# Optimization experiments

Measured on AMD Instinct MI355X. Metric: run time of the kernel, lower is better.

## Reference

```python
import jax, jax.numpy as jnp
import numpy as np

B, C_IN, H, W = 2, 256, 64, 64
C_OUT, NUM_HEADS = 256, 8
HEAD_DIM = C_OUT // NUM_HEADS


def setup_inputs() -> dict:
    key = jax.random.key(0)
    k_x, k_wqkv, k_bqkv, k_wout, k_bout = jax.random.split(key, 5)
    s_in = 1.0 / np.sqrt(C_IN)
    s_out = 1.0 / np.sqrt(C_OUT)
    return {
        "x": jax.random.normal(k_x, (B, C_IN, H, W), dtype=jnp.float32),
        "W_qkv": jax.random.uniform(k_wqkv, (C_IN, 3 * C_OUT), dtype=jnp.float32, minval=-s_in, maxval=s_in),
        "b_qkv": jax.random.uniform(k_bqkv, (3 * C_OUT,), dtype=jnp.float32, minval=-s_in, maxval=s_in),
        "W_out": jax.random.uniform(k_wout, (C_OUT, C_OUT), dtype=jnp.float32, minval=-s_out, maxval=s_out),
        "b_out": jax.random.uniform(k_bout, (C_OUT,), dtype=jnp.float32, minval=-s_out, maxval=s_out),
    }


def reference(x, W_qkv, b_qkv, W_out, b_out):
    b, c, h, w = x.shape
    n = h * w
    # [B, C, H, W] -> [B, N, C]
    xt = x.reshape(b, c, n).transpose(0, 2, 1)
    qkv = xt @ W_qkv + b_qkv                      # [B, N, 3*C_OUT]
    qkv = qkv.reshape(b, n, 3, NUM_HEADS, HEAD_DIM)
    q = qkv[:, :, 0].transpose(0, 2, 1, 3)        # [B, H, N, dh]
    k = qkv[:, :, 1].transpose(0, 2, 1, 3)
    v = qkv[:, :, 2].transpose(0, 2, 1, 3)
    scale = 1.0 / np.sqrt(HEAD_DIM).astype(np.float32)
    attn = jnp.einsum('bhnd,bhmd->bhnm', q, k) * scale   # [B, H, N, N]
    attn = jax.nn.softmax(attn, axis=-1)
    out = jnp.einsum('bhnm,bhmd->bhnd', attn, v)          # [B, H, N, dh]
    out = out.transpose(0, 2, 1, 3).reshape(b, n, C_OUT)  # [B, N, C_OUT]
    out = out @ W_out + b_out
    # [B, N, C_OUT] -> [B, C_OUT, sqrt(N), sqrt(N)]
    return out.transpose(0, 2, 1).reshape(b, C_OUT, h, w)
```

## Files before the change

kernel.cpp:

```cpp
#include <hip/hip_runtime.h>

typedef _Float16 f16;
typedef _Float16 f16x2 __attribute__((ext_vector_type(2)));
typedef _Float16 f16x4 __attribute__((ext_vector_type(4)));
typedef _Float16 f16x8 __attribute__((ext_vector_type(8)));
typedef float f32x4 __attribute__((ext_vector_type(4)));
typedef float f32x16 __attribute__((ext_vector_type(16)));

#define NTOK 4096
#define CIN  256
#define C3   768
#define CO   256
#define NH   8
#define DH   32

__device__ __forceinline__ f32x4 mfma16(f16x8 a, f16x8 b, f32x4 c) {
  return __builtin_amdgcn_mfma_f32_16x16x32_f16(a, b, c, 0, 0, 0);
}
__device__ __forceinline__ f32x16 mfma32(f16x8 a, f16x8 b, f32x16 c) {
  return __builtin_amdgcn_mfma_f32_32x32x16_f16(a, b, c, 0, 0, 0);
}

__device__ __forceinline__ float fexp2(float x) {
  float r; asm("v_exp_f32 %0, %1" : "=v"(r) : "v"(x)); return r;
}

__device__ __forceinline__ f16x2 cvt_pk(float lo, float hi) {
  return __builtin_bit_cast(f16x2, __builtin_amdgcn_cvt_pkrtz(lo, hi));
}

__device__ __forceinline__ f16x8 pack8(float a0, float a1, float a2, float a3,
                                       float a4, float a5, float a6, float a7) {
  f16x2 p0 = cvt_pk(a0, a1);
  f16x2 p1 = cvt_pk(a2, a3);
  f16x2 p2 = cvt_pk(a4, a5);
  f16x2 p3 = cvt_pk(a6, a7);
  f16x4 lo = __builtin_shufflevector(p0, p1, 0, 1, 2, 3);
  f16x4 hi = __builtin_shufflevector(p2, p3, 0, 1, 2, 3);
  return __builtin_shufflevector(lo, hi, 0, 1, 2, 3, 4, 5, 6, 7);
}

__device__ __forceinline__ f16x8 ld8(const f16* p) {
  f16x4 lo = *reinterpret_cast<const f16x4*>(p);
  f16x4 hi = *reinterpret_cast<const f16x4*>(p + 4);
  return __builtin_shufflevector(lo, hi, 0, 1, 2, 3, 4, 5, 6, 7);
}

__global__ __launch_bounds__(256) void qkv_kernel(
    const float* __restrict__ x, const float* __restrict__ Wqkv,
    const float* __restrict__ bqkv,
    f16* __restrict__ qbuf, f16* __restrict__ kbuf, f16* __restrict__ vbuf)
{
  __shared__ f16 As[64][36];
  __shared__ f16 Bs[64][36];
  const int b  = blockIdx.z;
  const int n0 = blockIdx.x * 64;
  const int j0 = blockIdx.y * 64;
  const int t  = threadIdx.x;
  const int w  = t >> 6;
  const int lane = t & 63;
  const int l16  = lane & 15;
  const int g4   = lane >> 4;
  const int rowi = t & 63;
  const int cg   = (t >> 6) * 8;

  f32x4 acc[4] = {};
  for (int k0 = 0; k0 < CIN; k0 += 32) {
    float av[8], bv[8];
#pragma unroll
    for (int jj = 0; jj < 8; ++jj) {
      av[jj] = x[((size_t)b * CIN + (k0 + cg + jj)) * NTOK + n0 + rowi];
      bv[jj] = Wqkv[(size_t)(k0 + cg + jj) * C3 + j0 + rowi];
    }
    f16x4 alo, ahi, blo, bhi;
#pragma unroll
    for (int jj = 0; jj < 4; ++jj) {
      alo[jj] = (f16)av[jj];  ahi[jj] = (f16)av[jj + 4];
      blo[jj] = (f16)bv[jj];  bhi[jj] = (f16)bv[jj + 4];
    }
    *reinterpret_cast<f16x4*>(&As[rowi][cg])     = alo;
    *reinterpret_cast<f16x4*>(&As[rowi][cg + 4]) = ahi;
    *reinterpret_cast<f16x4*>(&Bs[rowi][cg])     = blo;
    *reinterpret_cast<f16x4*>(&Bs[rowi][cg + 4]) = bhi;
    __syncthreads();
    f16x8 bf = ld8(&Bs[w * 16 + l16][g4 * 8]);
#pragma unroll
    for (int mf = 0; mf < 4; ++mf) {
      f16x8 af = ld8(&As[mf * 16 + l16][g4 * 8]);
      acc[mf] = mfma16(af, bf, acc[mf]);
    }
    __syncthreads();
  }
  const int j  = j0 + w * 16 + l16;
  const int s  = j >> 8;
  const int hh = (j >> 5) & 7;
  const int d  = j & 31;
  const float bias = bqkv[j];
  const float qscale = 0.25503472f;
  const int bh = b * NH + hh;
#pragma unroll
  for (int mf = 0; mf < 4; ++mf) {
#pragma unroll
    for (int r = 0; r < 4; ++r) {
      const int n = n0 + mf * 16 + g4 * 4 + r;
      const float v = acc[mf][r] + bias;
      if (s == 0) {
        qbuf[((size_t)bh * NTOK + n) * DH + d] = (f16)(v * qscale);
      } else if (s == 1) {
        kbuf[((size_t)bh * NTOK + n) * DH + d] = (f16)v;
      } else {
        const int g4p  = ((g4 & 1) << 1) | (g4 >> 1);
        const int tile = (n0 >> 5) + (mf >> 1);
        const int pos  = ((mf & 1) << 4) + g4p * 4 + r;
        vbuf[((size_t)bh * (NTOK / 32) + tile) * (DH * 32) + d * 32 + pos] = (f16)v;
      }
    }
  }
}

__global__ __launch_bounds__(512) void attn_kernel(
    const f16* __restrict__ qbuf, const f16* __restrict__ kbuf,
    const f16* __restrict__ vbuf, f16* __restrict__ ao)
{
  __shared__ float po_lds[4][32][33];
  __shared__ float pl_lds[4][32];

  const int flat = blockIdx.x + (int)gridDim.x * blockIdx.y;
  const int nper = ((int)gridDim.x * (int)gridDim.y) >> 3;
  const int jj   = (flat & 7) * nper + (flat >> 3);
  const int bh = jj >> 5;
  const int q0 = (jj & 31) * 128;
  const int b = bh >> 3, h = bh & 7;
  const int t = threadIdx.x, w = t >> 6, lane = t & 63;
  const int wq = w & 3, z = w >> 2;
  const int l32 = lane & 31, hi = lane >> 5;
  const size_t kbase = (size_t)bh * NTOK * DH;

  const int qrow = q0 + wq * 32 + l32;
  const f16* qp = qbuf + kbase + (size_t)qrow * DH + hi * 8;
  const f16x8 qf0 = *reinterpret_cast<const f16x8*>(qp);
  const f16x8 qf1 = *reinterpret_cast<const f16x8*>(qp + 16);

  const size_t zoff = (size_t)z * 65536;
  const f16* kp = kbuf + kbase + zoff + (size_t)l32 * DH + hi * 8;
  const f16* vp = vbuf + kbase + zoff + (size_t)l32 * 32 + hi * 8;

  f32x16 oacc = {};
  float lrun = 0.f;
  const f32x16 zero = {};

  f16x8 kna, knb, vca, vcb, vna, vnb;
  f32x16 scur;
  {
    f16x8 k0a = *reinterpret_cast<const f16x8*>(kp);
    f16x8 k0b = *reinterpret_cast<const f16x8*>(kp + 16);
    vca = *reinterpret_cast<const f16x8*>(vp);
    vcb = *reinterpret_cast<const f16x8*>(vp + 16);
    kna = *reinterpret_cast<const f16x8*>(kp + 1024);
    knb = *reinterpret_cast<const f16x8*>(kp + 1024 + 16);
    vna = *reinterpret_cast<const f16x8*>(vp + 1024);
    vnb = *reinterpret_cast<const f16x8*>(vp + 1024 + 16);
    scur = mfma32(k0a, qf0, zero);
    scur = mfma32(k0b, qf1, scur);
  }

  const f16* kfut = kp + 2048;
  const f16* vfut = vp + 2048;

#pragma unroll 2
  for (int tt = 0; tt < 64; ++tt) {
    f16x8 kpa = *reinterpret_cast<const f16x8*>(kfut);
    f16x8 kpb = *reinterpret_cast<const f16x8*>(kfut + 16);
    f16x8 vpa = *reinterpret_cast<const f16x8*>(vfut);
    f16x8 vpb = *reinterpret_cast<const f16x8*>(vfut + 16);
    kfut += 1024; vfut += 1024;

    __builtin_amdgcn_s_setprio(1);
    f32x16 snext = mfma32(kna, qf0, zero);
    snext = mfma32(knb, qf1, snext);
    __builtin_amdgcn_s_setprio(0);

    float e[16];
#pragma unroll
    for (int i = 0; i < 16; ++i) e[i] = fexp2(scur[i]);
    float a0 = e[0] + e[1],  a1 = e[2] + e[3];
    float a2 = e[4] + e[5],  a3 = e[6] + e[7];
    float a4 = e[8] + e[9],  a5 = e[10] + e[11];
    float a6 = e[12] + e[13], a7 = e[14] + e[15];
    lrun += ((a0 + a1) + (a2 + a3)) + ((a4 + a5) + (a6 + a7));

    f16x8 pb0 = pack8(e[0], e[1], e[2], e[3], e[4], e[5], e[6], e[7]);
    f16x8 pb1 = pack8(e[8], e[9], e[10], e[11], e[12], e[13], e[14], e[15]);

    __builtin_amdgcn_s_setprio(1);
    oacc = mfma32(vca, pb0, oacc);
    oacc = mfma32(vcb, pb1, oacc);
    __builtin_amdgcn_s_setprio(0);

    scur = snext;
    vca = vna; vcb = vnb;
    kna = kpa; knb = kpb;
    vna = vpa; vnb = vpb;
  }

  const float ltot = lrun + __shfl_xor(lrun, 32);

  if (z == 1) {
#pragma unroll
    for (int c4 = 0; c4 < 4; ++c4)
#pragma unroll
      for (int r = 0; r < 4; ++r)
        po_lds[wq][l32][hi * 4 + c4 * 8 + r] = oacc[c4 * 4 + r];
    if (hi == 0) pl_lds[wq][l32] = ltot;
  }
  __syncthreads();

  if (z == 0) {
    const float lt = ltot + pl_lds[wq][l32];
    const float inv = 1.0f / lt;
    f16* aop = (f16*)ao + ((size_t)b * NTOK + qrow) * CO + h * DH + hi * 4;
#pragma unroll
    for (int c4 = 0; c4 < 4; ++c4) {
      f16x4 st;
#pragma unroll
      for (int r = 0; r < 4; ++r)
        st[r] = (f16)((oacc[c4 * 4 + r] + po_lds[wq][l32][hi * 4 + c4 * 8 + r]) * inv);
      *reinterpret_cast<f16x4*>(aop + c4 * 8) = st;
    }
  }
}

__global__ __launch_bounds__(256) void proj_kernel(
    const f16* __restrict__ ao, const float* __restrict__ Wout,
    const float* __restrict__ bout, float* __restrict__ out)
{
  __shared__ f16 Ws[64][36];
  __shared__ f16 Aos[64][36];
  const int b  = blockIdx.z;
  const int n0 = blockIdx.x * 64;
  const int j0 = blockIdx.y * 64;
  const int t = threadIdx.x, w = t >> 6, lane = t & 63;
  const int l16 = lane & 15, g4 = lane >> 4;
  const int rowi = t & 63;
  const int cg   = (t >> 6) * 8;
  const int arow = t >> 2, aoff = (t & 3) * 8;
  f32x4 acc[4] = {};
  for (int k0 = 0; k0 < CO; k0 += 32) {
    float bv[8];
#pragma unroll
    for (int jj = 0; jj < 8; ++jj)
      bv[jj] = Wout[(size_t)(k0 + cg + jj) * CO + j0 + rowi];
    f16x8 a8 = *reinterpret_cast<const f16x8*>(
        ao + ((size_t)b * NTOK + n0 + arow) * CO + k0 + aoff);
    f16x4 blo, bhi;
#pragma unroll
    for (int jj = 0; jj < 4; ++jj) {
      blo[jj] = (f16)bv[jj];  bhi[jj] = (f16)bv[jj + 4];
    }
    *reinterpret_cast<f16x4*>(&Ws[rowi][cg])     = blo;
    *reinterpret_cast<f16x4*>(&Ws[rowi][cg + 4]) = bhi;
    f16x4 a8lo = __builtin_shufflevector(a8, a8, 0, 1, 2, 3);
    f16x4 a8hi = __builtin_shufflevector(a8, a8, 4, 5, 6, 7);
    *reinterpret_cast<f16x4*>(&Aos[arow][aoff])     = a8lo;
    *reinterpret_cast<f16x4*>(&Aos[arow][aoff + 4]) = a8hi;
    __syncthreads();
    f16x8 wf = ld8(&Ws[w * 16 + l16][g4 * 8]);
#pragma unroll
    for (int nf = 0; nf < 4; ++nf) {
      f16x8 af = ld8(&Aos[nf * 16 + l16][g4 * 8]);
      acc[nf] = mfma16(wf, af, acc[nf]);
    }
    __syncthreads();
  }
#pragma unroll
  for (int nf = 0; nf < 4; ++nf) {
#pragma unroll
    for (int r = 0; r < 4; ++r) {
      const int j = j0 + w * 16 + g4 * 4 + r;
      const int n = n0 + nf * 16 + l16;
      out[((size_t)b * CO + j) * NTOK + n] = acc[nf][r] + bout[j];
    }
  }
}

extern "C" void kernel_launch(void* const* d_in, const int* in_sizes, int n_in,
                              void* d_out, int out_size, void* d_ws, size_t ws_size,
                              hipStream_t stream) {
  const float* x    = (const float*)d_in[0];
  const float* Wqkv = (const float*)d_in[1];
  const float* bqkv = (const float*)d_in[2];
  const float* Wout = (const float*)d_in[3];
  const float* bout = (const float*)d_in[4];
  float* out = (float*)d_out;

  f16* qbuf = (f16*)d_ws;
  const size_t seg = (size_t)2 * NH * NTOK * DH;
  f16* kbuf = qbuf + seg;
  f16* vbuf = kbuf + seg;
  f16* ao   = vbuf + seg;

  qkv_kernel<<<dim3(NTOK / 64, C3 / 64, 2), 256, 0, stream>>>(x, Wqkv, bqkv, qbuf, kbuf, vbuf);
  attn_kernel<<<dim3(NTOK / 128, 16), 512, 0, stream>>>(qbuf, kbuf, vbuf, ao);
  proj_kernel<<<dim3(NTOK / 64, CO / 64, 2), 256, 0, stream>>>(ao, Wout, bout, out);
}
```

Baseline: 93.60 us.

## Process two query tiles per wave to reuse K/V fragments in attention

Halves the attention block to 256 threads and has each wave compute two 32-row query tiles (A and B) against the same K/V fragments loaded from global memory. This halves the K/V global load traffic per query and gives more independent MFMA and exp work per wave to hide latency. In exchange, per-wave register use roughly doubles (two score and output accumulators), which may lower occupancy, and there are half as many waves per block.

```diff
diff --git a/kernel.cpp b/kernel.cpp
--- a/kernel.cpp
+++ b/kernel.cpp
@@ -118,12 +118,12 @@
   }
 }
 
-__global__ __launch_bounds__(512) void attn_kernel(
+__global__ __launch_bounds__(256) void attn_kernel(
     const f16* __restrict__ qbuf, const f16* __restrict__ kbuf,
     const f16* __restrict__ vbuf, f16* __restrict__ ao)
 {
-  __shared__ float po_lds[4][32][33];
-  __shared__ float pl_lds[4][32];
+  __shared__ float po_lds[2][64][33];
+  __shared__ float pl_lds[2][64];
 
   const int flat = blockIdx.x + (int)gridDim.x * blockIdx.y;
   const int nper = ((int)gridDim.x * (int)gridDim.y) >> 3;
@@ -132,25 +132,29 @@
   const int q0 = (jj & 31) * 128;
   const int b = bh >> 3, h = bh & 7;
   const int t = threadIdx.x, w = t >> 6, lane = t & 63;
-  const int wq = w & 3, z = w >> 2;
+  const int wq = w & 1, z = w >> 1;
   const int l32 = lane & 31, hi = lane >> 5;
   const size_t kbase = (size_t)bh * NTOK * DH;
 
-  const int qrow = q0 + wq * 32 + l32;
-  const f16* qp = qbuf + kbase + (size_t)qrow * DH + hi * 8;
-  const f16x8 qf0 = *reinterpret_cast<const f16x8*>(qp);
-  const f16x8 qf1 = *reinterpret_cast<const f16x8*>(qp + 16);
+  const int qrowA = q0 + wq * 64 + l32;
+  const int qrowB = qrowA + 32;
+  const f16* qpA = qbuf + kbase + (size_t)qrowA * DH + hi * 8;
+  const f16* qpB = qbuf + kbase + (size_t)qrowB * DH + hi * 8;
+  const f16x8 qfA0 = *reinterpret_cast<const f16x8*>(qpA);
+  const f16x8 qfA1 = *reinterpret_cast<const f16x8*>(qpA + 16);
+  const f16x8 qfB0 = *reinterpret_cast<const f16x8*>(qpB);
+  const f16x8 qfB1 = *reinterpret_cast<const f16x8*>(qpB + 16);
 
   const size_t zoff = (size_t)z * 65536;
   const f16* kp = kbuf + kbase + zoff + (size_t)l32 * DH + hi * 8;
   const f16* vp = vbuf + kbase + zoff + (size_t)l32 * 32 + hi * 8;
 
-  f32x16 oacc = {};
-  float lrun = 0.f;
+  f32x16 oaccA = {}, oaccB = {};
+  float lrunA = 0.f, lrunB = 0.f;
   const f32x16 zero = {};
 
   f16x8 kna, knb, vca, vcb, vna, vnb;
-  f32x16 scur;
+  f32x16 scurA, scurB;
   {
     f16x8 k0a = *reinterpret_cast<const f16x8*>(kp);
     f16x8 k0b = *reinterpret_cast<const f16x8*>(kp + 16);
@@ -160,8 +164,10 @@
     knb = *reinterpret_cast<const f16x8*>(kp + 1024 + 16);
     vna = *reinterpret_cast<const f16x8*>(vp + 1024);
     vnb = *reinterpret_cast<const f16x8*>(vp + 1024 + 16);
-    scur = mfma32(k0a, qf0, zero);
-    scur = mfma32(k0b, qf1, scur);
+    scurA = mfma32(k0a, qfA0, zero);
+    scurA = mfma32(k0b, qfA1, scurA);
+    scurB = mfma32(k0a, qfB0, zero);
+    scurB = mfma32(k0b, qfB1, scurB);
   }
 
   const f16* kfut = kp + 2048;
@@ -176,56 +182,84 @@
     kfut += 1024; vfut += 1024;
 
     __builtin_amdgcn_s_setprio(1);
-    f32x16 snext = mfma32(kna, qf0, zero);
-    snext = mfma32(knb, qf1, snext);
+    f32x16 snextA = mfma32(kna, qfA0, zero);
+    snextA = mfma32(knb, qfA1, snextA);
+    f32x16 snextB = mfma32(kna, qfB0, zero);
+    snextB = mfma32(knb, qfB1, snextB);
     __builtin_amdgcn_s_setprio(0);
 
-    float e[16];
-#pragma unroll
-    for (int i = 0; i < 16; ++i) e[i] = fexp2(scur[i]);
-    float a0 = e[0] + e[1],  a1 = e[2] + e[3];
-    float a2 = e[4] + e[5],  a3 = e[6] + e[7];
-    float a4 = e[8] + e[9],  a5 = e[10] + e[11];
-    float a6 = e[12] + e[13], a7 = e[14] + e[15];
-    lrun += ((a0 + a1) + (a2 + a3)) + ((a4 + a5) + (a6 + a7));
-
-    f16x8 pb0 = pack8(e[0], e[1], e[2], e[3], e[4], e[5], e[6], e[7]);
-    f16x8 pb1 = pack8(e[8], e[9], e[10], e[11], e[12], e[13], e[14], e[15]);
+    float eA[16];
+#pragma unroll
+    for (int i = 0; i < 16; ++i) eA[i] = fexp2(scurA[i]);
+    {
+      float a0 = eA[0] + eA[1],  a1 = eA[2] + eA[3];
+      float a2 = eA[4] + eA[5],  a3 = eA[6] + eA[7];
+      float a4 = eA[8] + eA[9],  a5 = eA[10] + eA[11];
+      float a6 = eA[12] + eA[13], a7 = eA[14] + eA[15];
+      lrunA += ((a0 + a1) + (a2 + a3)) + ((a4 + a5) + (a6 + a7));
+    }
+    f16x8 pbA0 = pack8(eA[0], eA[1], eA[2], eA[3], eA[4], eA[5], eA[6], eA[7]);
+    f16x8 pbA1 = pack8(eA[8], eA[9], eA[10], eA[11], eA[12], eA[13], eA[14], eA[15]);
+
+    float eB[16];
+#pragma unroll
+    for (int i = 0; i < 16; ++i) eB[i] = fexp2(scurB[i]);
+    {
+      float a0 = eB[0] + eB[1],  a1 = eB[2] + eB[3];
+      float a2 = eB[4] + eB[5],  a3 = eB[6] + eB[7];
+      float a4 = eB[8] + eB[9],  a5 = eB[10] + eB[11];
+      float a6 = eB[12] + eB[13], a7 = eB[14] + eB[15];
+      lrunB += ((a0 + a1) + (a2 + a3)) + ((a4 + a5) + (a6 + a7));
+    }
+    f16x8 pbB0 = pack8(eB[0], eB[1], eB[2], eB[3], eB[4], eB[5], eB[6], eB[7]);
+    f16x8 pbB1 = pack8(eB[8], eB[9], eB[10], eB[11], eB[12], eB[13], eB[14], eB[15]);
 
     __builtin_amdgcn_s_setprio(1);
-    oacc = mfma32(vca, pb0, oacc);
-    oacc = mfma32(vcb, pb1, oacc);
+    oaccA = mfma32(vca, pbA0, oaccA);
+    oaccA = mfma32(vcb, pbA1, oaccA);
+    oaccB = mfma32(vca, pbB0, oaccB);
+    oaccB = mfma32(vcb, pbB1, oaccB);
     __builtin_amdgcn_s_setprio(0);
 
-    scur = snext;
+    scurA = snextA; scurB = snextB;
     vca = vna; vcb = vnb;
     kna = kpa; knb = kpb;
     vna = vpa; vnb = vpb;
   }
 
-  const float ltot = lrun + __shfl_xor(lrun, 32);
+  const float ltotA = lrunA + __shfl_xor(lrunA, 32);
+  const float ltotB = lrunB + __shfl_xor(lrunB, 32);
 
   if (z == 1) {
 #pragma unroll
     for (int c4 = 0; c4 < 4; ++c4)
 #pragma unroll
-      for (int r = 0; r < 4; ++r)
-        po_lds[wq][l32][hi * 4 + c4 * 8 + r] = oacc[c4 * 4 + r];
-    if (hi == 0) pl_lds[wq][l32] = ltot;
+      for (int r = 0; r < 4; ++r) {
+        po_lds[wq][l32][hi * 4 + c4 * 8 + r]      = oaccA[c4 * 4 + r];
+        po_lds[wq][32 + l32][hi * 4 + c4 * 8 + r] = oaccB[c4 * 4 + r];
+      }
+    if (hi == 0) {
+      pl_lds[wq][l32]      = ltotA;
+      pl_lds[wq][32 + l32] = ltotB;
+    }
   }
   __syncthreads();
 
   if (z == 0) {
-    const float lt = ltot + pl_lds[wq][l32];
-    const float inv = 1.0f / lt;
-    f16* aop = (f16*)ao + ((size_t)b * NTOK + qrow) * CO + h * DH + hi * 4;
+    const float invA = 1.0f / (ltotA + pl_lds[wq][l32]);
+    const float invB = 1.0f / (ltotB + pl_lds[wq][32 + l32]);
+    f16* aopA = (f16*)ao + ((size_t)b * NTOK + qrowA) * CO + h * DH + hi * 4;
+    f16* aopB = (f16*)ao + ((size_t)b * NTOK + qrowB) * CO + h * DH + hi * 4;
 #pragma unroll
     for (int c4 = 0; c4 < 4; ++c4) {
-      f16x4 st;
-#pragma unroll
-      for (int r = 0; r < 4; ++r)
-        st[r] = (f16)((oacc[c4 * 4 + r] + po_lds[wq][l32][hi * 4 + c4 * 8 + r]) * inv);
-      *reinterpret_cast<f16x4*>(aop + c4 * 8) = st;
+      f16x4 stA, stB;
+#pragma unroll
+      for (int r = 0; r < 4; ++r) {
+        stA[r] = (f16)((oaccA[c4 * 4 + r] + po_lds[wq][l32][hi * 4 + c4 * 8 + r]) * invA);
+        stB[r] = (f16)((oaccB[c4 * 4 + r] + po_lds[wq][32 + l32][hi * 4 + c4 * 8 + r]) * invB);
+      }
+      *reinterpret_cast<f16x4*>(aopA + c4 * 8) = stA;
+      *reinterpret_cast<f16x4*>(aopB + c4 * 8) = stB;
     }
   }
 }
@@ -300,6 +334,6 @@
   f16* ao   = vbuf + seg;
 
   qkv_kernel<<<dim3(NTOK / 64, C3 / 64, 2), 256, 0, stream>>>(x, Wqkv, bqkv, qbuf, kbuf, vbuf);
-  attn_kernel<<<dim3(NTOK / 128, 16), 512, 0, stream>>>(qbuf, kbuf, vbuf, ao);
+  attn_kernel<<<dim3(NTOK / 128, 16), 256, 0, stream>>>(qbuf, kbuf, vbuf, ao);
   proj_kernel<<<dim3(NTOK / 64, CO / 64, 2), 256, 0, stream>>>(ao, Wout, bout, out);
 }
```

Result: faster. 77.63 us (-17.1%).
